# Optimization experiments

Hardware: AMD Instinct MI355X
Metric: run time of the kernel (lower is better)

## Reference

```python
import jax, jax.numpy as jnp
import numpy as np
from jax import lax

NUM_HOP = 2      # opt.num_hop
POOL_HOP = 1     # Encoder(..., num_hop=1) in gnn_pools
K_POOL = 1024    # int(pooling_ratio * num_patches) = 0.5 * 2048
TH = 0.0         # opt.nonzero_th
T = 0.07         # NCE temperature
NEG_FILL = -10.0


def l2norm(x):
    # Normalize(power=2): x / (sum(x^2, dim=1, keepdim)^(1/2))
    return x / jnp.sqrt(jnp.sum(x * x, axis=1, keepdims=True))


def tagconv(A, h, W, b, k):
    # DGL TAGConv: concat_{i=0..k} (D^-1/2 A D^-1/2)^i h, then linear
    deg = jnp.sum(A, axis=1)
    dinv = lax.rsqrt(jnp.maximum(deg, 1e-12))
    An = A * dinv[:, None] * dinv[None, :]   # [N,N] normalized adjacency
    feats = [h]
    for _ in range(k):
        h = An @ h
        feats.append(h)
    return jnp.concatenate(feats, axis=1) @ W + b


def nce_pair(f_t, f_s):
    # calc_gnn NCE: positives = diag(f_t . f_s); negatives = full gram with diag masked to -10
    n = f_t.shape[0]
    eye = jnp.eye(n, dtype=bool)
    pos = jnp.sum(f_t * f_s, axis=1, keepdims=True)          # [N,1]
    neg_s = jnp.where(eye, NEG_FILL, f_t @ f_s.T)            # [N,N]
    neg_t = jnp.where(eye, NEG_FILL, f_s @ f_t.T)
    out_s = jnp.concatenate([pos, neg_s], axis=1) / T
    out_t = jnp.concatenate([pos, neg_t], axis=1) / T
    # CrossEntropy with label 0 == -log_softmax(out)[:, 0], mean over rows
    loss_s = -jnp.mean(jax.nn.log_softmax(out_s, axis=1)[:, 0])
    loss_t = -jnp.mean(jax.nn.log_softmax(out_t, axis=1)[:, 0])
    return loss_s + loss_t


def setup_inputs() -> dict:
    key = jax.random.key(0)
    ks = jax.random.split(key, 8)
    N, C, D = 2048, 512, 128
    g = 0.02  # init_gain ('normal' init)
    return {
        "fs": jax.random.normal(ks[0], (N, C), jnp.float32),
        "ft": jax.random.normal(ks[1], (N, C), jnp.float32),
        "W_embed": g * jax.random.normal(ks[2], (C, D), jnp.float32),
        "b_embed": jnp.zeros((D,), jnp.float32),
        "W_gnn": g * jax.random.normal(ks[3], ((NUM_HOP + 1) * D, D), jnp.float32),
        "b_gnn": jnp.zeros((D,), jnp.float32),
        "W_pool": g * jax.random.normal(ks[4], (D, 1), jnp.float32),
        "b_pool": jnp.zeros((1,), jnp.float32),
        "W_gnnp": g * jax.random.normal(ks[5], ((POOL_HOP + 1) * D, D), jnp.float32),
        "b_gnnp": jnp.zeros((D,), jnp.float32),
    }


def reference(fs, ft, W_embed, b_embed, W_gnn, b_gnn, W_pool, b_pool, W_gnnp, b_gnnp):
    # Embed: linear + l2 norm
    f_es = l2norm(fs @ W_embed + b_embed)   # student [N, nc]
    f_et = l2norm(ft @ W_embed + b_embed)   # teacher [N, nc]

    # nonzero_graph on detached teacher features; same adjacency reused for student
    ft_d = lax.stop_gradient(f_et)
    n = f_et.shape[0]
    eye = jnp.eye(n, dtype=bool)
    A = (ft_d @ ft_d.T > TH).astype(f_et.dtype)
    A = jnp.where(eye, 1.0, A)  # dgl.add_self_loop

    # TAGConv encoder + l2norm; teacher branch detached
    f_gt = lax.stop_gradient(l2norm(tagconv(A, f_et, W_gnn, b_gnn, NUM_HOP)))
    f_gs = l2norm(tagconv(A, f_es, W_gnn, b_gnn, NUM_HOP))
    loss_g = nce_pair(f_gt, f_gs)

    # Pool / top_k_graph
    scores = jax.nn.sigmoid((f_gt @ W_pool + b_pool)[:, 0])   # [N]
    vals, idx = lax.top_k(scores, K_POOL)
    new_ht = f_gt[idx] * vals[:, None]
    new_hs = f_gs[idx] * vals[:, None]
    un = (A > 0).astype(A.dtype)
    un2 = ((un @ un) > 0).astype(A.dtype)        # 2-hop boolean adjacency
    sub = un2[idx][:, idx]                       # [k,k]
    deg = jnp.sum(sub, axis=1)
    g_pool = sub / deg[None, :]                  # replicates torch broadcast in norm_g(g/degrees)

    # pooled-stage Encoder (TAGConv k=1) on the pooled graph structure (with self loops)
    k = K_POOL
    eye_k = jnp.eye(k, dtype=bool)
    Ap = (g_pool > 0).astype(A.dtype)
    Ap = jnp.where(eye_k, 1.0, Ap)
    f_pt = lax.stop_gradient(l2norm(tagconv(Ap, new_ht, W_gnnp, b_gnnp, POOL_HOP)))
    f_ps = l2norm(tagconv(Ap, new_hs, W_gnnp, b_gnnp, POOL_HOP))
    loss_pool = nce_pair(f_pt, f_ps)

    return loss_g + loss_pool
```

## Files before the change

kernel.cpp:

```cpp
#include <hip/hip_runtime.h>


#define TINV (1.0f / 0.07f)

using short8 = __attribute__((ext_vector_type(8))) short;
using f32x4  = __attribute__((ext_vector_type(4))) float;

__device__ __forceinline__ unsigned short f2bf(float f) {
    unsigned u = __float_as_uint(f);
    u += 0x7fff + ((u >> 16) & 1);
    return (unsigned short)(u >> 16);
}
__device__ __forceinline__ float bf2f(unsigned short h) {
    return __uint_as_float((unsigned)h << 16);
}
__device__ __forceinline__ void splitbf(float f, unsigned short& h, unsigned short& l) {
    h = f2bf(f);
    l = f2bf(f - bf2f(h));
}

__device__ __forceinline__ void mm64x128(const unsigned short* __restrict__ Ab, int lda,
                                         const unsigned short* __restrict__ Bb, int ldb,
                                         int i0, int j0, int k0, int Kc,
                                         f32x4 (&acc)[8],
                                         unsigned short (&As)[64][40],
                                         unsigned short (&Bs)[128][40])
{
    const int tid = threadIdx.x;
    const int w = tid >> 6;
    const int lane = tid & 63;
    const int m = lane & 15;
    const int q = lane >> 4;
    const int ar = tid >> 2;
    const int ac = (tid & 3) * 8;
    for (int ks = 0; ks < Kc; ks += 32) {
        const int k = k0 + ks;
        *(ulonglong2*)&As[ar][ac] =
            *(const ulonglong2*)(Ab + (size_t)(i0 + ar) * lda + k + ac);
        *(ulonglong2*)&Bs[ar][ac] =
            *(const ulonglong2*)(Bb + (size_t)(j0 + ar) * ldb + k + ac);
        *(ulonglong2*)&Bs[ar + 64][ac] =
            *(const ulonglong2*)(Bb + (size_t)(j0 + ar + 64) * ldb + k + ac);
        __syncthreads();
        short8 a = *(const short8*)&As[w * 16 + m][q * 8];
#pragma unroll
        for (int nt = 0; nt < 8; ++nt) {
            short8 b = *(const short8*)&Bs[nt * 16 + m][q * 8];
            acc[nt] = __builtin_amdgcn_mfma_f32_16x16x32_bf16(a, b, acc[nt], 0, 0, 0);
        }
        __syncthreads();
    }
}

__launch_bounds__(256)
__global__ void k_setup_embed(const float* __restrict__ fs, const float* __restrict__ ft,
                              const float* __restrict__ W, float* __restrict__ part,
                              size_t zstr, int* __restrict__ zwords, int zcount,
                              float* __restrict__ out,
                              const float* __restrict__ Wg, const float* __restrict__ Wp,
                              unsigned short* __restrict__ Wtall)
{
    __shared__ unsigned short Ah[64][40];
    __shared__ unsigned short Al[64][40];
    __shared__ unsigned short Bh[128][40];
    __shared__ unsigned short Bl[128][40];
    const int b = blockIdx.x;
    const int tid = threadIdx.x;
    if (b < 256) {
        const int z = b & 3;
        const int my = b >> 2;
        const float* A = (my < 32) ? ft : fs;
        const int i0 = (my & 31) * 64;
        const int w = tid >> 6, lane = tid & 63, m = lane & 15, q = lane >> 4;
        const int ar = tid >> 2, ac = (tid & 3) * 8;
        const int wkk = tid >> 3, wc0 = (tid & 7) * 16;
        f32x4 acc[8];
#pragma unroll
        for (int t = 0; t < 8; ++t)
#pragma unroll
            for (int r = 0; r < 4; ++r) acc[t][r] = 0.0f;
        for (int ks = 0; ks < 128; ks += 32) {
            const int k = z * 128 + ks;
            {
                float4 f1 = *(const float4*)(A + (size_t)(i0 + ar) * 512 + k + ac);
                float4 f2 = *(const float4*)(A + (size_t)(i0 + ar) * 512 + k + ac + 4);
                unsigned short h[8], l[8];
                splitbf(f1.x, h[0], l[0]); splitbf(f1.y, h[1], l[1]);
                splitbf(f1.z, h[2], l[2]); splitbf(f1.w, h[3], l[3]);
                splitbf(f2.x, h[4], l[4]); splitbf(f2.y, h[5], l[5]);
                splitbf(f2.z, h[6], l[6]); splitbf(f2.w, h[7], l[7]);
#pragma unroll
                for (int j = 0; j < 8; ++j) { Ah[ar][ac + j] = h[j]; Al[ar][ac + j] = l[j]; }
            }
            {
                const float* Wr = W + (size_t)(k + wkk) * 128 + wc0;
#pragma unroll
                for (int jj = 0; jj < 4; ++jj) {
                    float4 f = *(const float4*)(Wr + jj * 4);
                    unsigned short h, l;
                    splitbf(f.x, h, l); Bh[wc0 + jj*4 + 0][wkk] = h; Bl[wc0 + jj*4 + 0][wkk] = l;
                    splitbf(f.y, h, l); Bh[wc0 + jj*4 + 1][wkk] = h; Bl[wc0 + jj*4 + 1][wkk] = l;
                    splitbf(f.z, h, l); Bh[wc0 + jj*4 + 2][wkk] = h; Bl[wc0 + jj*4 + 2][wkk] = l;
                    splitbf(f.w, h, l); Bh[wc0 + jj*4 + 3][wkk] = h; Bl[wc0 + jj*4 + 3][wkk] = l;
                }
            }
            __syncthreads();
            short8 ah = *(const short8*)&Ah[w * 16 + m][q * 8];
            short8 al = *(const short8*)&Al[w * 16 + m][q * 8];
#pragma unroll
            for (int nt = 0; nt < 8; ++nt) {
                short8 bh = *(const short8*)&Bh[nt * 16 + m][q * 8];
                short8 bl = *(const short8*)&Bl[nt * 16 + m][q * 8];
                acc[nt] = __builtin_amdgcn_mfma_f32_16x16x32_bf16(ah, bh, acc[nt], 0, 0, 0);
                acc[nt] = __builtin_amdgcn_mfma_f32_16x16x32_bf16(ah, bl, acc[nt], 0, 0, 0);
                acc[nt] = __builtin_amdgcn_mfma_f32_16x16x32_bf16(al, bh, acc[nt], 0, 0, 0);
            }
            __syncthreads();
        }
        float* dst = part + (size_t)z * zstr;
#pragma unroll
        for (int nt = 0; nt < 8; ++nt) {
            const int col = nt * 16 + m;
#pragma unroll
            for (int r = 0; r < 4; ++r) {
                const int row = my * 64 + w * 16 + q * 4 + r;
                dst[(size_t)row * 128 + col] = acc[nt][r];
            }
        }
    } else if (b < 305) {
        const int i = (b - 256) * 256 + tid;
        if (i < zcount) zwords[i] = 0;
        if (b == 256 && tid == 0) out[0] = 0.0f;
    } else {
        const int e0 = (b - 305) * 2048 + tid;
#pragma unroll
        for (int it = 0; it < 8; ++it) {
            const int e = e0 + it * 256;
            const int c = e >> 14;
            const int rem = e & 16383;
            const int n = rem >> 7, k = rem & 127;
            const float* src = (c < 3) ? (Wg + (size_t)c * 16384)
                                       : (Wp + (size_t)(c - 3) * 16384);
            Wtall[e] = f2bf(src[(size_t)k * 128 + n]);
        }
    }
}

__global__ void combine_norm(const float* __restrict__ part, int nz, size_t zstr,
                             const float* __restrict__ bias,
                             unsigned short* __restrict__ bfh,
                             unsigned short* __restrict__ bfl)
{
    const int row = blockIdx.x;
    const int tid = threadIdx.x;
    float v = bias[tid];
    for (int z = 0; z < nz; ++z) v += part[(size_t)z * zstr + (size_t)row * 128 + tid];
    __shared__ float red[128];
    red[tid] = v * v;
    __syncthreads();
    for (int s = 64; s > 0; s >>= 1) {
        if (tid < s) red[tid] += red[tid + s];
        __syncthreads();
    }
    const float o = v * (1.0f / sqrtf(red[0]));
    unsigned short h, l;
    splitbf(o, h, l);
    bfh[(size_t)row * 128 + tid] = h;
    bfl[(size_t)row * 128 + tid] = l;
}

__launch_bounds__(256)
__global__ void k_gram_fused(const unsigned short* __restrict__ febh,
                             const unsigned short* __restrict__ febl,
                             unsigned short* __restrict__ A01,
                             unsigned long long* __restrict__ bits,
                             int* __restrict__ deg,
                             const unsigned short* __restrict__ Wt,
                             float* __restrict__ hW)
{
    __shared__ __align__(16) unsigned char smem[25600];
    const int b = blockIdx.x;
    const int tid = threadIdx.x;
    if (b >= 528) {
        unsigned short (&As2)[64][40]  = *reinterpret_cast<unsigned short(*)[64][40]>(smem);
        unsigned short (&Bs2)[128][40] = *reinterpret_cast<unsigned short(*)[128][40]>(smem + 5120);
        const int lb = b - 528;
        const int z = lb >> 6;
        const int i0 = (lb & 63) * 64;
        f32x4 acc[8];
#pragma unroll
        for (int t = 0; t < 8; ++t)
#pragma unroll
            for (int r = 0; r < 4; ++r) acc[t][r] = 0.0f;
        mm64x128(febh, 128, Wt + (size_t)z * 16384, 128, i0, 0, 0, 128, acc, As2, Bs2);
        const int w = tid >> 6, lane = tid & 63, m = lane & 15, q = lane >> 4;
        float* Cb = hW + (size_t)z * (4096ull * 128);
#pragma unroll
        for (int nt = 0; nt < 8; ++nt) {
            const int col = nt * 16 + m;
#pragma unroll
            for (int r = 0; r < 4; ++r) {
                const int row = i0 + w * 16 + q * 4 + r;
                Cb[(size_t)row * 128 + col] = acc[nt][r];
            }
        }
        return;
    }
    unsigned short (&Ah)[64][40] = *reinterpret_cast<unsigned short(*)[64][40]>(smem);
    unsigned short (&Al)[64][40] = *reinterpret_cast<unsigned short(*)[64][40]>(smem + 5120);
    unsigned short (&Bh)[64][40] = *reinterpret_cast<unsigned short(*)[64][40]>(smem + 10240);
    unsigned short (&Bl)[64][40] = *reinterpret_cast<unsigned short(*)[64][40]>(smem + 15360);
    unsigned char (&predB)[64][64] = *reinterpret_cast<unsigned char(*)[64][64]>(smem + 20480);
    unsigned long long (&chk)[64]  = *reinterpret_cast<unsigned long long(*)[64]>(smem + 24576);
    unsigned long long (&chkT)[64] = *reinterpret_cast<unsigned long long(*)[64]>(smem + 25088);
    int by = (int)((sqrtf(8.0f * b + 1.0f) - 1.0f) * 0.5f);
    while ((by + 1) * (by + 2) / 2 <= b) ++by;
    while (by * (by + 1) / 2 > b) --by;
    const int bx = b - by * (by + 1) / 2;
    const int i0 = by * 64, j0 = bx * 64;
    const int w = tid >> 6, lane = tid & 63, m = lane & 15, q = lane >> 4;
    const int ar = tid >> 2, ac = (tid & 3) * 8;
    f32x4 acc[4];
#pragma unroll
    for (int t = 0; t < 4; ++t)
#pragma unroll
        for (int r = 0; r < 4; ++r) acc[t][r] = 0.0f;
    for (int ks = 0; ks < 128; ks += 32) {
        *(ulonglong2*)&Ah[ar][ac] = *(const ulonglong2*)(febh + (size_t)(i0 + ar) * 128 + ks + ac);
        *(ulonglong2*)&Al[ar][ac] = *(const ulonglong2*)(febl + (size_t)(i0 + ar) * 128 + ks + ac);
        *(ulonglong2*)&Bh[ar][ac] = *(const ulonglong2*)(febh + (size_t)(j0 + ar) * 128 + ks + ac);
        *(ulonglong2*)&Bl[ar][ac] = *(const ulonglong2*)(febl + (size_t)(j0 + ar) * 128 + ks + ac);
        __syncthreads();
        short8 ah = *(const short8*)&Ah[w * 16 + m][q * 8];
        short8 al = *(const short8*)&Al[w * 16 + m][q * 8];
#pragma unroll
        for (int nt = 0; nt < 4; ++nt) {
            short8 bh = *(const short8*)&Bh[nt * 16 + m][q * 8];
            short8 bl = *(const short8*)&Bl[nt * 16 + m][q * 8];
            acc[nt] = __builtin_amdgcn_mfma_f32_16x16x32_bf16(ah, bh, acc[nt], 0, 0, 0);
            acc[nt] = __builtin_amdgcn_mfma_f32_16x16x32_bf16(ah, bl, acc[nt], 0, 0, 0);
            acc[nt] = __builtin_amdgcn_mfma_f32_16x16x32_bf16(al, bh, acc[nt], 0, 0, 0);
        }
        __syncthreads();
    }
#pragma unroll
    for (int nt = 0; nt < 4; ++nt) {
        const int lc = nt * 16 + m;
#pragma unroll
        for (int r = 0; r < 4; ++r) {
            const int lr = w * 16 + q * 4 + r;
            bool pred = (acc[nt][r] > 0.0f) || (i0 + lr == j0 + lc);
            predB[lr][lc] = pred ? 1 : 0;
        }
    }
    __syncthreads();
    if (tid < 64) {
        unsigned long long c = 0;
        const unsigned* rowp = (const unsigned*)predB[tid];
#pragma unroll
        for (int t = 0; t < 16; ++t) {
            unsigned u = rowp[t];
            c |= (unsigned long long)((u >> 0) & 1) << (4 * t + 0);
            c |= (unsigned long long)((u >> 8) & 1) << (4 * t + 1);
            c |= (unsigned long long)((u >> 16) & 1) << (4 * t + 2);
            c |= (unsigned long long)((u >> 24) & 1) << (4 * t + 3);
        }
        chk[tid] = c;
        bits[(size_t)(i0 + tid) * 32 + (j0 >> 6)] = c;
        atomicAdd(&deg[i0 + tid], __popcll(c));
    } else if (tid < 128 && bx != by) {
        const int r = tid - 64;
        unsigned long long c = 0;
#pragma unroll
        for (int i = 0; i < 64; ++i)
            c |= (unsigned long long)(predB[i][r] & 1) << i;
        chkT[r] = c;
        bits[(size_t)(j0 + r) * 32 + (i0 >> 6)] = c;
        atomicAdd(&deg[j0 + r], __popcll(c));
    }
    __syncthreads();
#pragma unroll
    for (int it = 0; it < 4; ++it) {
        const int row = it * 16 + (tid >> 4);
        const int c0 = (tid & 15) * 4;
        unsigned short o[4];
#pragma unroll
        for (int c = 0; c < 4; ++c)
            o[c] = ((chk[row] >> (c0 + c)) & 1) ? (unsigned short)0x3F80 : (unsigned short)0;
        *(ulonglong1*)&A01[(size_t)(i0 + row) * 2048 + j0 + c0] = *(ulonglong1*)o;
        if (bx != by) {
            unsigned short o2[4];
#pragma unroll
            for (int c = 0; c < 4; ++c)
                o2[c] = ((chkT[row] >> (c0 + c)) & 1) ? (unsigned short)0x3F80 : (unsigned short)0;
            *(ulonglong1*)&A01[(size_t)(j0 + row) * 2048 + i0 + c0] = *(ulonglong1*)o2;
        }
    }
}

__launch_bounds__(256)
__global__ void mm_bf16(const unsigned short* __restrict__ A, int lda, size_t aZ,
                        const unsigned short* __restrict__ B, int ldb, size_t bZ,
                        float* __restrict__ C, int ldc, size_t cZ,
                        int Kc, int kZ)
{
    __shared__ unsigned short As[64][40];
    __shared__ unsigned short Bs[128][40];
    const int tid = threadIdx.x;
    const int bz = blockIdx.z;
    const int i0 = blockIdx.y * 64;
    const int j0 = blockIdx.x * 128;
    const int k0 = bz * kZ;
    const unsigned short* Ab = A + (size_t)bz * aZ;
    const unsigned short* Bb = B + (size_t)bz * bZ;
    float* Cb = C + (size_t)bz * cZ;
    f32x4 acc[8];
#pragma unroll
    for (int t = 0; t < 8; ++t)
#pragma unroll
        for (int r = 0; r < 4; ++r) acc[t][r] = 0.0f;
    mm64x128(Ab, lda, Bb, ldb, i0, j0, k0, Kc, acc, As, Bs);
    const int w = tid >> 6, lane = tid & 63, m = lane & 15, q = lane >> 4;
#pragma unroll
    for (int nt = 0; nt < 8; ++nt) {
        const int col = j0 + nt * 16 + m;
#pragma unroll
        for (int r = 0; r < 4; ++r) {
            const int row = i0 + w * 16 + q * 4 + r;
            Cb[(size_t)row * ldc + col] = acc[nt][r];
        }
    }
}

__global__ void reduce_xt(const float* __restrict__ part, int nz, size_t zstr,
                          int M, const float* __restrict__ dinv,
                          const float* __restrict__ addT,
                          unsigned short* __restrict__ xt)
{
    __shared__ float T[32][33];
    const int tid = threadIdx.x;
    const int iloc = tid >> 3, nq = (tid & 7) * 4;
    const int n = blockIdx.x * 32 + nq;
    const int i = blockIdx.y * 32 + iloc;
    float4 s = *(const float4*)(part + (size_t)i * 256 + n);
    for (int z = 1; z < nz; ++z) {
        float4 t = *(const float4*)(part + (size_t)z * zstr + (size_t)i * 256 + n);
        s.x += t.x; s.y += t.y; s.z += t.z; s.w += t.w;
    }
    const float d = dinv[i];
    const int srow = (n >= 128 ? M : 0) + i;
    float4 a = *(const float4*)(addT + (size_t)srow * 128 + (n & 127));
    T[nq + 0][iloc] = (a.x + s.x * d) * d;
    T[nq + 1][iloc] = (a.y + s.y * d) * d;
    T[nq + 2][iloc] = (a.z + s.z * d) * d;
    T[nq + 3][iloc] = (a.w + s.w * d) * d;
    __syncthreads();
    const int nloc = tid >> 3, ic = (tid & 7) * 4;
    unsigned short o2[4];
#pragma unroll
    for (int c = 0; c < 4; ++c) o2[c] = f2bf(T[nloc][ic + c]);
    *(ulonglong1*)(xt + (size_t)(blockIdx.x * 32 + nloc) * M + blockIdx.y * 32 + ic) =
        *(ulonglong1*)o2;
}

__global__ void combine_tag(const float* __restrict__ part, int nz, size_t zstr,
                            int Mnodes,
                            const float* __restrict__ add,
                            const float* __restrict__ dinv,
                            const float* __restrict__ bias,
                            float* __restrict__ f32out,
                            unsigned short* __restrict__ bf16out,
                            const float* __restrict__ Wp, const float* __restrict__ bp,
                            float* __restrict__ scores)
{
    const int row = blockIdx.x;
    const int tid = threadIdx.x;
    const int node = (row < Mnodes) ? row : row - Mnodes;
    const int boff = (row < Mnodes) ? 0 : 128;
    float s = 0.0f;
    for (int z = 0; z < nz; ++z)
        s += part[(size_t)z * zstr + (size_t)node * 256 + boff + tid];
    float v = bias[tid] + add[(size_t)row * 128 + tid] + dinv[node] * s;
    __shared__ float red[128];
    red[tid] = v * v;
    __syncthreads();
    for (int st = 64; st > 0; st >>= 1) {
        if (tid < st) red[tid] += red[tid + st];
        __syncthreads();
    }
    const float o = v * (1.0f / sqrtf(red[0]));
    if (f32out) f32out[(size_t)row * 128 + tid] = o;
    bf16out[(size_t)row * 128 + tid] = f2bf(o);
    if (Wp && row < Mnodes) {
        __syncthreads();
        red[tid] = o * Wp[tid];
        __syncthreads();
        for (int st = 64; st > 0; st >>= 1) {
            if (tid < st) red[tid] += red[tid + st];
            __syncthreads();
        }
        if (tid == 0) scores[row] = 1.0f / (1.0f + expf(-(red[0] + bp[0])));
    }
}

__global__ void make_xt(const float* __restrict__ src, const int* __restrict__ deg,
                        unsigned short* __restrict__ xt, float* __restrict__ dinv)
{
    __shared__ float T[32][33];
    const int b = blockIdx.x;
    const int bx = b & 7, by = b >> 3;
    const int tid = threadIdx.x;
    const int iloc = tid >> 3, nq = (tid & 7) * 4;
    const int n0 = bx * 32;
    const int i = by * 32 + iloc;
    const int srow = (n0 >= 128 ? 2048 : 0) + i;
    float4 f = *(const float4*)(src + (size_t)srow * 128 + ((n0 + nq) & 127));
    const float d = 1.0f / sqrtf((float)deg[i]);
    if (bx == 0 && (tid & 7) == 0) dinv[i] = d;
    T[nq + 0][iloc] = f.x * d; T[nq + 1][iloc] = f.y * d;
    T[nq + 2][iloc] = f.z * d; T[nq + 3][iloc] = f.w * d;
    __syncthreads();
    const int nloc = tid >> 3, ic = (tid & 7) * 4;
    unsigned short o[4];
#pragma unroll
    for (int c = 0; c < 4; ++c) o[c] = f2bf(T[nloc][ic + c]);
    *(ulonglong1*)(xt + (size_t)(n0 + nloc) * 2048 + by * 32 + ic) = *(ulonglong1*)o;
}

__launch_bounds__(256)
__global__ void k_nce_topk(const unsigned short* __restrict__ A,
                           const unsigned short* __restrict__ B,
                           float* __restrict__ rowsum, float* __restrict__ colsum,
                           float* __restrict__ pos, int gramBlocks, int bw,
                           const float* __restrict__ scores,
                           float* __restrict__ vals, int* __restrict__ idx)
{
    __shared__ unsigned short As[64][40];
    __shared__ unsigned short Bs[128][40];
    __shared__ float colbuf[4][128];
    __shared__ unsigned sv[2048];
    __shared__ int hist[256];
    __shared__ int shp, shr, sh_base, sh_out, wsum[5];
    const int tid = threadIdx.x;
    const int b = blockIdx.x;
    if (b < gramBlocks) {
        const int bx = b % bw, by = b / bw;
        const int i0 = by * 64;
        const int j0 = bx * 128;
        const int w = tid >> 6;
        const int lane = tid & 63;
        const int m = lane & 15;
        const int q = lane >> 4;
        f32x4 acc[8];
#pragma unroll
        for (int t = 0; t < 8; ++t)
#pragma unroll
            for (int r = 0; r < 4; ++r) acc[t][r] = 0.0f;
        mm64x128(A, 128, B, 128, i0, j0, 0, 128, acc, As, Bs);
        float rpart[4] = {0.0f, 0.0f, 0.0f, 0.0f};
        float cpart[8];
#pragma unroll
        for (int nt = 0; nt < 8; ++nt) {
            const int col = j0 + nt * 16 + m;
            float cs = 0.0f;
#pragma unroll
            for (int r = 0; r < 4; ++r) {
                const int row = i0 + w * 16 + q * 4 + r;
                float g = acc[nt][r];
                float e = __expf(g * TINV);
                if (row == col) { pos[row] = g; e = 0.0f; }
                rpart[r] += e;
                cs += e;
            }
            cpart[nt] = cs;
        }
#pragma unroll
        for (int r = 0; r < 4; ++r) {
            float v = rpart[r];
            v += __shfl_xor(v, 1); v += __shfl_xor(v, 2);
            v += __shfl_xor(v, 4); v += __shfl_xor(v, 8);
            if (m == 0) atomicAdd(&rowsum[i0 + w * 16 + q * 4 + r], v);
        }
#pragma unroll
        for (int nt = 0; nt < 8; ++nt) {
            float v = cpart[nt];
            v += __shfl_xor(v, 16); v += __shfl_xor(v, 32);
            if (q == 0) colbuf[w][nt * 16 + m] = v;
        }
        __syncthreads();
        if (tid < 128) {
            float v = colbuf[0][tid] + colbuf[1][tid] + colbuf[2][tid] + colbuf[3][tid];
            atomicAdd(&colsum[j0 + tid], v);
        }
    } else {
        for (int e = tid; e < 2048; e += 256) sv[e] = __float_as_uint(scores[e]);
        if (tid == 0) { shp = 0; shr = 1024; sh_base = 0; sh_out = 0; }
        __syncthreads();
        for (int byte = 3; byte >= 0; --byte) {
            hist[tid] = 0;
            __syncthreads();
            const unsigned pref = (unsigned)shp;
            const unsigned pmask = (byte == 3) ? 0u : (0xFFFFFFFFu << ((byte + 1) * 8));
            for (int e = tid; e < 2048; e += 256) {
                unsigned u = sv[e];
                if ((u & pmask) == (pref & pmask))
                    atomicAdd(&hist[(u >> (byte * 8)) & 255], 1);
            }
            __syncthreads();
            if (tid == 0) {
                int rem = shr, bs = 255;
                for (; bs > 0; --bs) {
                    if (hist[bs] >= rem) break;
                    rem -= hist[bs];
                }
                shp = (int)(pref | ((unsigned)bs << (byte * 8)));
                shr = rem;
            }
            __syncthreads();
        }
        const unsigned t = (unsigned)shp;
        const int remain = shr;
        const int lane = tid & 63, wave = tid >> 6;
        for (int pass = 0; pass < 8; ++pass) {
            const int e = pass * 256 + tid;
            const unsigned u = sv[e];
            const bool eq = (u == t);
            unsigned long long mk = __ballot(eq);
            int wpre = __popcll(mk & ((1ull << lane) - 1ull));
            if (lane == 0) wsum[wave] = __popcll(mk);
            __syncthreads();
            if (tid == 0) {
                int a = sh_base;
                for (int ww = 0; ww < 4; ++ww) { int c = wsum[ww]; wsum[ww] = a; a += c; }
                sh_base = a;
            }
            __syncthreads();
            const int rank = eq ? (wsum[wave] + wpre) : 0x7fffffff;
            if ((u > t) || (eq && rank < remain)) {
                int slot = atomicAdd(&sh_out, 1);
                idx[slot] = e;
                vals[slot] = __uint_as_float(u);
            }
            __syncthreads();
        }
    }
}

__global__ void k_final_ap(const float* __restrict__ rs, const float* __restrict__ cs,
                           const float* __restrict__ pos, float* __restrict__ out,
                           const unsigned long long* __restrict__ bits,
                           const int* __restrict__ idx,
                           unsigned short* __restrict__ Ap, int* __restrict__ degp)
{
    __shared__ unsigned long long pb[32][33];
    __shared__ unsigned long long qb[32][33];
    __shared__ float red[256];
    const int b = blockIdx.x;
    const int tid = threadIdx.x;
    if (b < 1024) {
        const int tp = (b >> 5) * 32;
        const int tq = (b & 31) * 32;
        for (int t = tid; t < 1024; t += 256) {
            int r = t >> 5, w = t & 31;
            pb[r][w] = bits[(size_t)idx[tp + r] * 32 + w];
            qb[r][w] = bits[(size_t)idx[tq + r] * 32 + w];
        }
        __syncthreads();
        const int pi = tid >> 3;
        const int qc0 = (tid & 7) * 4;
        unsigned long long a0 = 0, a1 = 0, a2 = 0, a3 = 0;
#pragma unroll
        for (int w = 0; w < 32; ++w) {
            const unsigned long long p = pb[pi][w];
            a0 |= p & qb[qc0 + 0][w];
            a1 |= p & qb[qc0 + 1][w];
            a2 |= p & qb[qc0 + 2][w];
            a3 |= p & qb[qc0 + 3][w];
        }
        unsigned short o[4] = { (unsigned short)(a0 ? 0x3F80 : 0),
                                (unsigned short)(a1 ? 0x3F80 : 0),
                                (unsigned short)(a2 ? 0x3F80 : 0),
                                (unsigned short)(a3 ? 0x3F80 : 0) };
        *(ulonglong1*)&Ap[(size_t)(tp + pi) * 1024 + tq + qc0] = *(ulonglong1*)o;
        int v = (a0 ? 1 : 0) + (a1 ? 1 : 0) + (a2 ? 1 : 0) + (a3 ? 1 : 0);
        v += __shfl_xor(v, 1); v += __shfl_xor(v, 2); v += __shfl_xor(v, 4);
        if ((tid & 7) == 0) atomicAdd(&degp[tp + pi], v);
    } else {
        const int i = (b - 1024) * 256 + tid;
        float p = pos[i] * TINV;
        float ep = __expf(p);
        float t = (logf(rs[i] + ep) - p) + (logf(cs[i] + ep) - p);
        red[tid] = t;
        __syncthreads();
        for (int s = 128; s > 0; s >>= 1) {
            if (tid < s) red[tid] += red[tid + s];
            __syncthreads();
        }
        if (tid == 0) atomicAdd(out, red[0] * (1.0f / 2048.0f));
    }
}

__global__ void nce_final(const float* __restrict__ rs, const float* __restrict__ cs,
                          const float* __restrict__ pos, float invN,
                          float* __restrict__ out)
{
    const int i = blockIdx.x * 256 + threadIdx.x;
    float p = pos[i] * TINV;
    float ep = __expf(p);
    float t = (logf(rs[i] + ep) - p) + (logf(cs[i] + ep) - p);
    __shared__ float red[256];
    red[threadIdx.x] = t;
    __syncthreads();
    for (int s = 128; s > 0; s >>= 1) {
        if (threadIdx.x < s) red[threadIdx.x] += red[threadIdx.x + s];
        __syncthreads();
    }
    if (threadIdx.x == 0) atomicAdd(out, red[0] * invN);
}

__global__ void gather_nh(const float* __restrict__ f_g, const int* __restrict__ idx,
                          const float* __restrict__ vals, const int* __restrict__ degp,
                          unsigned short* __restrict__ nhb, float* __restrict__ dinvp)
{
    const int b = blockIdx.x;
    const int tid = threadIdx.x;
    if (b < 4) {
        const int p2 = b * 256 + tid;
        dinvp[p2] = 1.0f / sqrtf((float)degp[p2]);
    }
    const int hrow = b * 8 + (tid >> 5);
    const int cq = (tid & 31) * 4;
    const int p = hrow & 1023;
    const int s = idx[p];
    const float v = vals[p];
    const int srow = (hrow >= 1024 ? 2048 : 0) + s;
    float4 f = *(const float4*)(f_g + (size_t)srow * 128 + cq);
    unsigned short o[4] = { f2bf(f.x * v), f2bf(f.y * v), f2bf(f.z * v), f2bf(f.w * v) };
    *(ulonglong1*)&nhb[(size_t)hrow * 128 + cq] = *(ulonglong1*)o;
}

__launch_bounds__(256)
__global__ void k_lin_pool(const unsigned short* __restrict__ nhb,
                           const unsigned short* __restrict__ WtP,
                           const float* __restrict__ dinvp,
                           float* __restrict__ P0,
                           unsigned short* __restrict__ Xtp)
{
    __shared__ unsigned short As[64][40];
    __shared__ unsigned short Bs[128][40];
    const int b = blockIdx.x;
    const int z = b >> 5;
    const int i0 = (b & 31) * 64;
    const int tid = threadIdx.x;
    f32x4 acc[8];
#pragma unroll
    for (int t = 0; t < 8; ++t)
#pragma unroll
        for (int r = 0; r < 4; ++r) acc[t][r] = 0.0f;
    mm64x128(nhb, 128, WtP + (size_t)z * 16384, 128, i0, 0, 0, 128, acc, As, Bs);
    const int w = tid >> 6, lane = tid & 63, m = lane & 15, q = lane >> 4;
    if (z == 0) {
#pragma unroll
        for (int nt = 0; nt < 8; ++nt) {
            const int col = nt * 16 + m;
#pragma unroll
            for (int r = 0; r < 4; ++r) {
                const int row = i0 + w * 16 + q * 4 + r;
                P0[(size_t)row * 128 + col] = acc[nt][r];
            }
        }
    } else {
        const int boff = (i0 >= 1024) ? 128 : 0;
        const int p0 = (i0 & 1023) + w * 16 + q * 4;
        float4 dv = *(const float4*)(dinvp + p0);
        const float dvr[4] = { dv.x, dv.y, dv.z, dv.w };
#pragma unroll
        for (int nt = 0; nt < 8; ++nt) {
            const int n = boff + nt * 16 + m;
            unsigned short o[4];
#pragma unroll
            for (int r = 0; r < 4; ++r) o[r] = f2bf(acc[nt][r] * dvr[r]);
            *(ulonglong1*)&Xtp[(size_t)n * 1024 + p0] = *(ulonglong1*)o;
        }
    }
}

extern "C" void kernel_launch(void* const* d_in, const int* in_sizes, int n_in,
                              void* d_out, int out_size, void* d_ws, size_t ws_size,
                              hipStream_t stream)
{
    (void)in_sizes; (void)n_in; (void)out_size; (void)ws_size;
    const float* fs      = (const float*)d_in[0];
    const float* ft      = (const float*)d_in[1];
    const float* W_embed = (const float*)d_in[2];
    const float* b_embed = (const float*)d_in[3];
    const float* W_gnn   = (const float*)d_in[4];
    const float* b_gnn   = (const float*)d_in[5];
    const float* W_pool  = (const float*)d_in[6];
    const float* b_pool  = (const float*)d_in[7];
    const float* W_gnnp  = (const float*)d_in[8];
    const float* b_gnnp  = (const float*)d_in[9];
    float* out = (float*)d_out;

    float* ws = (float*)d_ws;
    size_t o = 0;
    auto alloc = [&](size_t n) { float* p = ws + o; o += (n + 3) & ~3ull; return p; };
    float* bigB   = alloc(2048ull * 2048);
    float* f_g    = alloc(4096 * 128);
    unsigned short* A01  = (unsigned short*)alloc(2048ull * 2048 / 2);
    unsigned short* feb  = (unsigned short*)alloc(4096ull * 128 / 2);
    unsigned short* febl = (unsigned short*)alloc(4096ull * 128 / 2);
    unsigned short* Xt1  = (unsigned short*)alloc(256ull * 2048 / 2);
    unsigned short* Xt2  = (unsigned short*)alloc(256ull * 2048 / 2);
    unsigned short* f_gb = (unsigned short*)alloc(4096ull * 128 / 2);
    unsigned short* Wtall= (unsigned short*)alloc(5ull * 16384 / 2);
    unsigned short* Ap01 = (unsigned short*)alloc(1024ull * 1024 / 2);
    unsigned short* nhb  = (unsigned short*)alloc(2048ull * 128 / 2);
    unsigned short* Xtp  = (unsigned short*)alloc(256ull * 1024 / 2);
    unsigned short* f_pb = (unsigned short*)alloc(2048ull * 128 / 2);
    float* hW     = alloc(3ull * 4096 * 128);
    float* P0     = alloc(2048ull * 128);
    float* dinv   = alloc(2048);
    float* scores = alloc(2048);
    float* vals   = alloc(1024);
    int*   idxb   = (int*)alloc(1024);
    float* dinvp  = alloc(1024);
    unsigned long long* bits = (unsigned long long*)alloc(2048 * 32 * 2);
    float* nceb = alloc(9216);
    int*   deg  = (int*)alloc(2048);
    int*   degp = (int*)alloc(1024);
    const int kZeroCount = 9216 + 2048 + 1024;

    const size_t FSTR = 4096ull * 128;
    const size_t PSTR = 1024ull * 256;
    unsigned short* Wt  = Wtall;
    unsigned short* WtP = Wtall + 3ull * 16384;
    float* hW0 = hW;
    float* hW1 = hW + FSTR;
    float* hW2 = hW + 2 * FSTR;
    float* rs  = nceb;
    float* csu = nceb + 2048;
    float* pos = nceb + 4096;
    float* rsp  = nceb + 6144;
    float* csp  = nceb + 7168;
    float* posp = nceb + 8192;

    k_setup_embed<<<345, 256, 0, stream>>>(fs, ft, W_embed, bigB, FSTR,
                                           (int*)nceb, kZeroCount, out, W_gnn, W_gnnp, Wtall);
    combine_norm<<<4096, 128, 0, stream>>>(bigB, 4, FSTR, b_embed, feb, febl);
    k_gram_fused<<<720, 256, 0, stream>>>(feb, febl, A01, bits, deg, Wt, hW);
    make_xt<<<512, 256, 0, stream>>>(hW2, deg, Xt1, dinv);
    mm_bf16<<<dim3(2, 32, 4), 256, 0, stream>>>(A01, 2048, 0, Xt1, 2048, 0,
                                                bigB, 256, FSTR, 512, 512);
    reduce_xt<<<dim3(8, 64), 256, 0, stream>>>(bigB, 4, FSTR, 2048, dinv, hW1, Xt2);
    mm_bf16<<<dim3(2, 32, 4), 256, 0, stream>>>(A01, 2048, 0, Xt2, 2048, 0,
                                                bigB, 256, FSTR, 512, 512);
    combine_tag<<<4096, 128, 0, stream>>>(bigB, 4, FSTR, 2048, hW0, dinv, b_gnn,
                                          f_g, f_gb, W_pool, b_pool, scores);
    k_nce_topk<<<513, 256, 0, stream>>>(f_gb, f_gb + 2048 * 128, rs, csu, pos,
                                        512, 16, scores, vals, idxb);
    k_final_ap<<<1032, 256, 0, stream>>>(rs, csu, pos, out, bits, idxb, Ap01, degp);
    gather_nh<<<256, 256, 0, stream>>>(f_g, idxb, vals, degp, nhb, dinvp);
    k_lin_pool<<<64, 256, 0, stream>>>(nhb, WtP, dinvp, P0, Xtp);
    mm_bf16<<<dim3(2, 16, 4), 256, 0, stream>>>(Ap01, 1024, 0, Xtp, 1024, 0,
                                                bigB, 256, PSTR, 256, 256);
    combine_tag<<<2048, 128, 0, stream>>>(bigB, 4, PSTR, 1024, P0, dinvp, b_gnnp,
                                          nullptr, f_pb, nullptr, nullptr, nullptr);
    k_nce_topk<<<128, 256, 0, stream>>>(f_pb, f_pb + 1024 * 128, rsp, csp, posp,
                                        128, 8, nullptr, nullptr, nullptr);
    nce_final<<<4, 256, 0, stream>>>(rsp, csp, posp, 1.0f / 1024.0f, out);
}
```

Baseline: 201.6 us.

## Prefetch GEMM tiles into registers and fuse pool gather and NCE final into neighbours

The shared GEMM helper and the embed kernel now load the next K-slice into registers while MFMAs run on the current slice, hiding global latency. The separate gather_nh kernel is folded into k_lin_pool, which gathers, scales and converts rows on the fly and computes dinvp itself. nce_final is removed by having the last block of the pooled k_nce_topk do the loss reduction, using an atomic counter and threadfence. Together these cut two launches and one intermediate buffer, at the cost of extra registers and a last-block serial tail.

```diff
diff --git a/kernel.cpp b/kernel.cpp
--- a/kernel.cpp
+++ b/kernel.cpp
@@ -33,15 +33,22 @@
     const int q = lane >> 4;
     const int ar = tid >> 2;
     const int ac = (tid & 3) * 8;
+    const unsigned short* Apt = Ab + (size_t)(i0 + ar) * lda + k0 + ac;
+    const unsigned short* Bpt0 = Bb + (size_t)(j0 + ar) * ldb + k0 + ac;
+    const unsigned short* Bpt1 = Bb + (size_t)(j0 + ar + 64) * ldb + k0 + ac;
+    ulonglong2 ra  = *(const ulonglong2*)Apt;
+    ulonglong2 rb0 = *(const ulonglong2*)Bpt0;
+    ulonglong2 rb1 = *(const ulonglong2*)Bpt1;
     for (int ks = 0; ks < Kc; ks += 32) {
-        const int k = k0 + ks;
-        *(ulonglong2*)&As[ar][ac] =
-            *(const ulonglong2*)(Ab + (size_t)(i0 + ar) * lda + k + ac);
-        *(ulonglong2*)&Bs[ar][ac] =
-            *(const ulonglong2*)(Bb + (size_t)(j0 + ar) * ldb + k + ac);
-        *(ulonglong2*)&Bs[ar + 64][ac] =
-            *(const ulonglong2*)(Bb + (size_t)(j0 + ar + 64) * ldb + k + ac);
-        __syncthreads();
+        *(ulonglong2*)&As[ar][ac] = ra;
+        *(ulonglong2*)&Bs[ar][ac] = rb0;
+        *(ulonglong2*)&Bs[ar + 64][ac] = rb1;
+        __syncthreads();
+        if (ks + 32 < Kc) {
+            ra  = *(const ulonglong2*)(Apt + ks + 32);
+            rb0 = *(const ulonglong2*)(Bpt0 + ks + 32);
+            rb1 = *(const ulonglong2*)(Bpt1 + ks + 32);
+        }
         short8 a = *(const short8*)&As[w * 16 + m][q * 8];
 #pragma unroll
         for (int nt = 0; nt < 8; ++nt) {
@@ -74,37 +81,57 @@
         const int w = tid >> 6, lane = tid & 63, m = lane & 15, q = lane >> 4;
         const int ar = tid >> 2, ac = (tid & 3) * 8;
         const int wkk = tid >> 3, wc0 = (tid & 7) * 16;
+        const float* Apt = A + (size_t)(i0 + ar) * 512 + z * 128 + ac;
+        const float* Wpt = W + (size_t)(z * 128 + wkk) * 128 + wc0;
+        float4 fa0 = *(const float4*)(Apt);
+        float4 fa1 = *(const float4*)(Apt + 4);
+        float4 fw0 = *(const float4*)(Wpt);
+        float4 fw1 = *(const float4*)(Wpt + 4);
+        float4 fw2 = *(const float4*)(Wpt + 8);
+        float4 fw3 = *(const float4*)(Wpt + 12);
         f32x4 acc[8];
 #pragma unroll
         for (int t = 0; t < 8; ++t)
 #pragma unroll
             for (int r = 0; r < 4; ++r) acc[t][r] = 0.0f;
         for (int ks = 0; ks < 128; ks += 32) {
-            const int k = z * 128 + ks;
             {
-                float4 f1 = *(const float4*)(A + (size_t)(i0 + ar) * 512 + k + ac);
-                float4 f2 = *(const float4*)(A + (size_t)(i0 + ar) * 512 + k + ac + 4);
                 unsigned short h[8], l[8];
-                splitbf(f1.x, h[0], l[0]); splitbf(f1.y, h[1], l[1]);
-                splitbf(f1.z, h[2], l[2]); splitbf(f1.w, h[3], l[3]);
-                splitbf(f2.x, h[4], l[4]); splitbf(f2.y, h[5], l[5]);
-                splitbf(f2.z, h[6], l[6]); splitbf(f2.w, h[7], l[7]);
+                splitbf(fa0.x, h[0], l[0]); splitbf(fa0.y, h[1], l[1]);
+                splitbf(fa0.z, h[2], l[2]); splitbf(fa0.w, h[3], l[3]);
+                splitbf(fa1.x, h[4], l[4]); splitbf(fa1.y, h[5], l[5]);
+                splitbf(fa1.z, h[6], l[6]); splitbf(fa1.w, h[7], l[7]);
 #pragma unroll
                 for (int j = 0; j < 8; ++j) { Ah[ar][ac + j] = h[j]; Al[ar][ac + j] = l[j]; }
             }
             {
-                const float* Wr = W + (size_t)(k + wkk) * 128 + wc0;
-#pragma unroll
-                for (int jj = 0; jj < 4; ++jj) {
-                    float4 f = *(const float4*)(Wr + jj * 4);
-                    unsigned short h, l;
-                    splitbf(f.x, h, l); Bh[wc0 + jj*4 + 0][wkk] = h; Bl[wc0 + jj*4 + 0][wkk] = l;
-                    splitbf(f.y, h, l); Bh[wc0 + jj*4 + 1][wkk] = h; Bl[wc0 + jj*4 + 1][wkk] = l;
-                    splitbf(f.z, h, l); Bh[wc0 + jj*4 + 2][wkk] = h; Bl[wc0 + jj*4 + 2][wkk] = l;
-                    splitbf(f.w, h, l); Bh[wc0 + jj*4 + 3][wkk] = h; Bl[wc0 + jj*4 + 3][wkk] = l;
-                }
-            }
-            __syncthreads();
+                unsigned short h, l;
+                splitbf(fw0.x, h, l); Bh[wc0 + 0][wkk] = h; Bl[wc0 + 0][wkk] = l;
+                splitbf(fw0.y, h, l); Bh[wc0 + 1][wkk] = h; Bl[wc0 + 1][wkk] = l;
+                splitbf(fw0.z, h, l); Bh[wc0 + 2][wkk] = h; Bl[wc0 + 2][wkk] = l;
+                splitbf(fw0.w, h, l); Bh[wc0 + 3][wkk] = h; Bl[wc0 + 3][wkk] = l;
+                splitbf(fw1.x, h, l); Bh[wc0 + 4][wkk] = h; Bl[wc0 + 4][wkk] = l;
+                splitbf(fw1.y, h, l); Bh[wc0 + 5][wkk] = h; Bl[wc0 + 5][wkk] = l;
+                splitbf(fw1.z, h, l); Bh[wc0 + 6][wkk] = h; Bl[wc0 + 6][wkk] = l;
+                splitbf(fw1.w, h, l); Bh[wc0 + 7][wkk] = h; Bl[wc0 + 7][wkk] = l;
+                splitbf(fw2.x, h, l); Bh[wc0 + 8][wkk] = h; Bl[wc0 + 8][wkk] = l;
+                splitbf(fw2.y, h, l); Bh[wc0 + 9][wkk] = h; Bl[wc0 + 9][wkk] = l;
+                splitbf(fw2.z, h, l); Bh[wc0 + 10][wkk] = h; Bl[wc0 + 10][wkk] = l;
+                splitbf(fw2.w, h, l); Bh[wc0 + 11][wkk] = h; Bl[wc0 + 11][wkk] = l;
+                splitbf(fw3.x, h, l); Bh[wc0 + 12][wkk] = h; Bl[wc0 + 12][wkk] = l;
+                splitbf(fw3.y, h, l); Bh[wc0 + 13][wkk] = h; Bl[wc0 + 13][wkk] = l;
+                splitbf(fw3.z, h, l); Bh[wc0 + 14][wkk] = h; Bl[wc0 + 14][wkk] = l;
+                splitbf(fw3.w, h, l); Bh[wc0 + 15][wkk] = h; Bl[wc0 + 15][wkk] = l;
+            }
+            __syncthreads();
+            if (ks + 32 < 128) {
+                fa0 = *(const float4*)(Apt + ks + 32);
+                fa1 = *(const float4*)(Apt + ks + 32 + 4);
+                fw0 = *(const float4*)(Wpt + (size_t)(ks + 32) * 128);
+                fw1 = *(const float4*)(Wpt + (size_t)(ks + 32) * 128 + 4);
+                fw2 = *(const float4*)(Wpt + (size_t)(ks + 32) * 128 + 8);
+                fw3 = *(const float4*)(Wpt + (size_t)(ks + 32) * 128 + 12);
+            }
             short8 ah = *(const short8*)&Ah[w * 16 + m][q * 8];
             short8 al = *(const short8*)&Al[w * 16 + m][q * 8];
 #pragma unroll
@@ -433,7 +460,9 @@
                            float* __restrict__ rowsum, float* __restrict__ colsum,
                            float* __restrict__ pos, int gramBlocks, int bw,
                            const float* __restrict__ scores,
-                           float* __restrict__ vals, int* __restrict__ idx)
+                           float* __restrict__ vals, int* __restrict__ idx,
+                           int* __restrict__ counter, float* __restrict__ outT,
+                           float invN, int nRows)
 {
     __shared__ unsigned short As[64][40];
     __shared__ unsigned short Bs[128][40];
@@ -441,6 +470,7 @@
     __shared__ unsigned sv[2048];
     __shared__ int hist[256];
     __shared__ int shp, shr, sh_base, sh_out, wsum[5];
+    __shared__ int lastFlag;
     const int tid = threadIdx.x;
     const int b = blockIdx.x;
     if (b < gramBlocks) {
@@ -491,6 +521,29 @@
         if (tid < 128) {
             float v = colbuf[0][tid] + colbuf[1][tid] + colbuf[2][tid] + colbuf[3][tid];
             atomicAdd(&colsum[j0 + tid], v);
+        }
+        if (counter) {
+            __threadfence();
+            __syncthreads();
+            if (tid == 0) lastFlag = (atomicAdd(counter, 1) == gramBlocks - 1);
+            __syncthreads();
+            if (lastFlag) {
+                __threadfence();
+                float accl = 0.0f;
+                for (int i = tid; i < nRows; i += 256) {
+                    float p = pos[i] * TINV;
+                    float ep = __expf(p);
+                    accl += (logf(rowsum[i] + ep) - p) + (logf(colsum[i] + ep) - p);
+                }
+                float* red = (float*)colbuf;
+                red[tid] = accl;
+                __syncthreads();
+                for (int s = 128; s > 0; s >>= 1) {
+                    if (tid < s) red[tid] += red[tid + s];
+                    __syncthreads();
+                }
+                if (tid == 0) atomicAdd(outT, red[0] * invN);
+            }
         }
     } else {
         for (int e = tid; e < 2048; e += 256) sv[e] = __float_as_uint(scores[e]);
@@ -600,51 +653,12 @@
     }
 }
 
-__global__ void nce_final(const float* __restrict__ rs, const float* __restrict__ cs,
-                          const float* __restrict__ pos, float invN,
-                          float* __restrict__ out)
-{
-    const int i = blockIdx.x * 256 + threadIdx.x;
-    float p = pos[i] * TINV;
-    float ep = __expf(p);
-    float t = (logf(rs[i] + ep) - p) + (logf(cs[i] + ep) - p);
-    __shared__ float red[256];
-    red[threadIdx.x] = t;
-    __syncthreads();
-    for (int s = 128; s > 0; s >>= 1) {
-        if (threadIdx.x < s) red[threadIdx.x] += red[threadIdx.x + s];
-        __syncthreads();
-    }
-    if (threadIdx.x == 0) atomicAdd(out, red[0] * invN);
-}
-
-__global__ void gather_nh(const float* __restrict__ f_g, const int* __restrict__ idx,
-                          const float* __restrict__ vals, const int* __restrict__ degp,
-                          unsigned short* __restrict__ nhb, float* __restrict__ dinvp)
-{
-    const int b = blockIdx.x;
-    const int tid = threadIdx.x;
-    if (b < 4) {
-        const int p2 = b * 256 + tid;
-        dinvp[p2] = 1.0f / sqrtf((float)degp[p2]);
-    }
-    const int hrow = b * 8 + (tid >> 5);
-    const int cq = (tid & 31) * 4;
-    const int p = hrow & 1023;
-    const int s = idx[p];
-    const float v = vals[p];
-    const int srow = (hrow >= 1024 ? 2048 : 0) + s;
-    float4 f = *(const float4*)(f_g + (size_t)srow * 128 + cq);
-    unsigned short o[4] = { f2bf(f.x * v), f2bf(f.y * v), f2bf(f.z * v), f2bf(f.w * v) };
-    *(ulonglong1*)&nhb[(size_t)hrow * 128 + cq] = *(ulonglong1*)o;
-}
-
 __launch_bounds__(256)
-__global__ void k_lin_pool(const unsigned short* __restrict__ nhb,
+__global__ void k_lin_pool(const float* __restrict__ f_g, const int* __restrict__ idx,
+                           const float* __restrict__ vals, const int* __restrict__ degp,
                            const unsigned short* __restrict__ WtP,
-                           const float* __restrict__ dinvp,
-                           float* __restrict__ P0,
-                           unsigned short* __restrict__ Xtp)
+                           float* __restrict__ P0, unsigned short* __restrict__ Xtp,
+                           float* __restrict__ dinvp)
 {
     __shared__ unsigned short As[64][40];
     __shared__ unsigned short Bs[128][40];
@@ -652,13 +666,41 @@
     const int z = b >> 5;
     const int i0 = (b & 31) * 64;
     const int tid = threadIdx.x;
+    const int w = tid >> 6, lane = tid & 63, m = lane & 15, q = lane >> 4;
+    const int ar = tid >> 2, ac = (tid & 3) * 8;
+    const int hrow = i0 + ar;
+    const int p = hrow & 1023;
+    const int s = idx[p];
+    const float v = vals[p];
+    const size_t srow = (size_t)((hrow >= 1024) ? 2048 : 0) + s;
+    const int br = tid >> 1, bc = (tid & 1) * 16;
     f32x4 acc[8];
 #pragma unroll
     for (int t = 0; t < 8; ++t)
 #pragma unroll
         for (int r = 0; r < 4; ++r) acc[t][r] = 0.0f;
-    mm64x128(nhb, 128, WtP + (size_t)z * 16384, 128, i0, 0, 0, 128, acc, As, Bs);
-    const int w = tid >> 6, lane = tid & 63, m = lane & 15, q = lane >> 4;
+    for (int ks = 0; ks < 128; ks += 32) {
+        float4 f1 = *(const float4*)(f_g + srow * 128 + ks + ac);
+        float4 f2 = *(const float4*)(f_g + srow * 128 + ks + ac + 4);
+        short8 pk;
+        pk[0] = (short)f2bf(f1.x * v); pk[1] = (short)f2bf(f1.y * v);
+        pk[2] = (short)f2bf(f1.z * v); pk[3] = (short)f2bf(f1.w * v);
+        pk[4] = (short)f2bf(f2.x * v); pk[5] = (short)f2bf(f2.y * v);
+        pk[6] = (short)f2bf(f2.z * v); pk[7] = (short)f2bf(f2.w * v);
+        *(short8*)&As[ar][ac] = pk;
+        *(ulonglong2*)&Bs[br][bc] =
+            *(const ulonglong2*)(WtP + (size_t)z * 16384 + (size_t)br * 128 + ks + bc);
+        *(ulonglong2*)&Bs[br][bc + 8] =
+            *(const ulonglong2*)(WtP + (size_t)z * 16384 + (size_t)br * 128 + ks + bc + 8);
+        __syncthreads();
+        short8 a = *(const short8*)&As[w * 16 + m][q * 8];
+#pragma unroll
+        for (int nt = 0; nt < 8; ++nt) {
+            short8 bb = *(const short8*)&Bs[nt * 16 + m][q * 8];
+            acc[nt] = __builtin_amdgcn_mfma_f32_16x16x32_bf16(a, bb, acc[nt], 0, 0, 0);
+        }
+        __syncthreads();
+    }
     if (z == 0) {
 #pragma unroll
         for (int nt = 0; nt < 8; ++nt) {
@@ -672,8 +714,13 @@
     } else {
         const int boff = (i0 >= 1024) ? 128 : 0;
         const int p0 = (i0 & 1023) + w * 16 + q * 4;
-        float4 dv = *(const float4*)(dinvp + p0);
-        const float dvr[4] = { dv.x, dv.y, dv.z, dv.w };
+        int4 dg = *(const int4*)(degp + p0);
+        const float dvr[4] = { rsqrtf((float)dg.x), rsqrtf((float)dg.y),
+                               rsqrtf((float)dg.z), rsqrtf((float)dg.w) };
+        if (i0 < 1024 && m == 0) {
+            dinvp[p0 + 0] = dvr[0]; dinvp[p0 + 1] = dvr[1];
+            dinvp[p0 + 2] = dvr[2]; dinvp[p0 + 3] = dvr[3];
+        }
 #pragma unroll
         for (int nt = 0; nt < 8; ++nt) {
             const int n = boff + nt * 16 + m;
@@ -715,7 +762,6 @@
     unsigned short* f_gb = (unsigned short*)alloc(4096ull * 128 / 2);
     unsigned short* Wtall= (unsigned short*)alloc(5ull * 16384 / 2);
     unsigned short* Ap01 = (unsigned short*)alloc(1024ull * 1024 / 2);
-    unsigned short* nhb  = (unsigned short*)alloc(2048ull * 128 / 2);
     unsigned short* Xtp  = (unsigned short*)alloc(256ull * 1024 / 2);
     unsigned short* f_pb = (unsigned short*)alloc(2048ull * 128 / 2);
     float* hW     = alloc(3ull * 4096 * 128);
@@ -729,7 +775,8 @@
     float* nceb = alloc(9216);
     int*   deg  = (int*)alloc(2048);
     int*   degp = (int*)alloc(1024);
-    const int kZeroCount = 9216 + 2048 + 1024;
+    int*   cnt  = (int*)alloc(4);
+    const int kZeroCount = 9216 + 2048 + 1024 + 4;
 
     const size_t FSTR = 4096ull * 128;
     const size_t PSTR = 1024ull * 256;
@@ -758,15 +805,15 @@
     combine_tag<<<4096, 128, 0, stream>>>(bigB, 4, FSTR, 2048, hW0, dinv, b_gnn,
                                           f_g, f_gb, W_pool, b_pool, scores);
     k_nce_topk<<<513, 256, 0, stream>>>(f_gb, f_gb + 2048 * 128, rs, csu, pos,
-                                        512, 16, scores, vals, idxb);
+                                        512, 16, scores, vals, idxb,
+                                        nullptr, nullptr, 0.0f, 0);
     k_final_ap<<<1032, 256, 0, stream>>>(rs, csu, pos, out, bits, idxb, Ap01, degp);
-    gather_nh<<<256, 256, 0, stream>>>(f_g, idxb, vals, degp, nhb, dinvp);
-    k_lin_pool<<<64, 256, 0, stream>>>(nhb, WtP, dinvp, P0, Xtp);
+    k_lin_pool<<<64, 256, 0, stream>>>(f_g, idxb, vals, degp, WtP, P0, Xtp, dinvp);
     mm_bf16<<<dim3(2, 16, 4), 256, 0, stream>>>(Ap01, 1024, 0, Xtp, 1024, 0,
                                                 bigB, 256, PSTR, 256, 256);
     combine_tag<<<2048, 128, 0, stream>>>(bigB, 4, PSTR, 1024, P0, dinvp, b_gnnp,
                                           nullptr, f_pb, nullptr, nullptr, nullptr);
     k_nce_topk<<<128, 256, 0, stream>>>(f_pb, f_pb + 1024 * 128, rsp, csp, posp,
-                                        128, 8, nullptr, nullptr, nullptr);
-    nce_final<<<4, 256, 0, stream>>>(rsp, csp, posp, 1.0f / 1024.0f, out);
-}
+                                        128, 8, nullptr, nullptr, nullptr,
+                                        cnt, out, 1.0f / 1024.0f, 1024);
+}
```

Measured after the change: 202.9 us. About the same (+0.6%).
